# Performance work log

Measured on AMD Instinct MI355X. Metric: run time of the kernel, lower is better.

## Reference

```python
import jax, jax.numpy as jnp
import numpy as np

B = 524288
D_IN = 128
D_OUT = 128
MASK_DENSITY = 0.25  # fraction of DAG edges present


def setup_inputs() -> dict:
    key = jax.random.key(0)
    k = jax.random.split(key, 6)
    x0 = jax.random.normal(k[0], (B, D_IN), dtype=jnp.float32)
    x1 = jax.random.normal(k[1], (B, D_IN), dtype=jnp.float32)
    # weights ~ N(0, 0.1^2) as in torch.normal(mean=0, std=0.1)
    w0 = jax.random.normal(k[2], (D_OUT, D_IN), dtype=jnp.float32) * 0.1
    w1 = jax.random.normal(k[3], (D_OUT, D_IN), dtype=jnp.float32) * 0.1
    # binary DAG connectivity masks [out_dim, in_dims[i]]
    m0 = (jax.random.uniform(k[4], (D_OUT, D_IN)) < MASK_DENSITY).astype(jnp.float32)
    m1 = (jax.random.uniform(k[5], (D_OUT, D_IN)) < MASK_DENSITY).astype(jnp.float32)
    return {"x0": x0, "x1": x1, "w0": w0, "w1": w1, "m0": m0, "m1": m1}


def reference(x0, x1, w0, w1, m0, m1):
    # sum_i  x_i @ (W_i * M_i)^T   -> [B, out_dim]
    # (note: original module creates self.bias but never adds it in forward)
    out = jnp.einsum("bi,oi->bo", x0, w0 * m0)
    out = out + jnp.einsum("bi,oi->bo", x1, w1 * m1)
    return out
```

## Files before the change

### kernel.cpp

```cpp
#include <hip/hip_runtime.h>

typedef __attribute__((ext_vector_type(4))) float f32x4;
typedef __attribute__((ext_vector_type(4))) int   i32x4;
typedef __attribute__((ext_vector_type(2))) unsigned int u32x2;

#define NBLK 512
#define NTHR 512
#define NT   32
#define DOUT 128

__device__ __forceinline__ unsigned short bf_rne(float x) {
  unsigned u = __builtin_bit_cast(unsigned, x);
  return (unsigned short)((u + 0x7FFFu + ((u >> 16) & 1u)) >> 16);
}
__device__ __forceinline__ void split2(float x, short& hi, short& lo) {
  unsigned u = __builtin_bit_cast(unsigned, x);
  float hf = __builtin_bit_cast(float, u & 0xFFFF0000u);
  hi = (short)(unsigned short)(u >> 16);
  lo = (short)bf_rne(x - hf);
}
__device__ __forceinline__ unsigned cvtpk(float a, float b) {
  unsigned r;
  asm("v_cvt_pk_bf16_f32 %0, %1, %2" : "=v"(r) : "v"(a), "v"(b));
  return r;
}
__device__ __forceinline__ void gll16(const float* g, char* l) {
  __builtin_amdgcn_global_load_lds(
      (const __attribute__((address_space(1))) unsigned int*)g,
      (__attribute__((address_space(3))) unsigned int*)l, 16, 0, 0);
}
#define MFMA_AW(ACC, W, X)                                                   \
  asm("s_nop 1\n\tv_mfma_f32_16x16x32_bf16 %0, %1, %2, %0"                   \
      : "+v"(ACC) : "a"(W), "v"(X))

__global__ __launch_bounds__(NTHR, 2)
void dagmm(const float* __restrict__ x0, const float* __restrict__ x1,
           const float* __restrict__ w0, const float* __restrict__ w1,
           const float* __restrict__ m0, const float* __restrict__ m1,
           float* __restrict__ out)
{
  __shared__ __align__(16) char L[98304];
  const int t   = threadIdx.x;
  const int l   = t & 63;
  const int w   = t >> 6;
  const int l16 = l & 15;
  const int lq  = l >> 4;

  i32x4 WH[8], WL[8];
  {
    const int col = w * 16 + l16;
#pragma unroll
    for (int ks = 0; ks < 8; ++ks) {
      const int k0 = ks * 32 + lq * 8;
      const float* wp = (k0 < 128) ? (w0 + col * 128 + k0) : (w1 + col * 128 + (k0 - 128));
      const float* mp = (k0 < 128) ? (m0 + col * 128 + k0) : (m1 + col * 128 + (k0 - 128));
      float4 wa = *(const float4*)wp, wb = *(const float4*)(wp + 4);
      float4 ma = *(const float4*)mp, mb = *(const float4*)(mp + 4);
      float v[8] = {wa.x*ma.x, wa.y*ma.y, wa.z*ma.z, wa.w*ma.w,
                    wb.x*mb.x, wb.y*mb.y, wb.z*mb.z, wb.w*mb.w};
      short hv[8], lv[8];
#pragma unroll
      for (int j = 0; j < 8; ++j) split2(v[j], hv[j], lv[j]);
      WH[ks] = *(const i32x4*)hv;
      WL[ks] = *(const i32x4*)lv;
      asm volatile("" : "+a"(WH[ks]));
      asm volatile("" : "+a"(WL[ks]));
    }
  }

  const size_t Tbase = (size_t)blockIdx.x * (NT * 32);
  const float* xsrc = (l < 32) ? (x0 + l * 4) : (x1 + (l - 32) * 4);

#define ISSUE(ts, r)                                                         \
  {                                                                          \
    _Pragma("unroll")                                                        \
    for (int i = 0; i < 4; ++i) {                                            \
      const int row = w * 4 + i;                                             \
      const size_t grow = Tbase + (size_t)(ts) * 32 + row;                   \
      gll16(xsrc + grow * 128, L + (r) * 32768 + row * 1024);                \
    }                                                                        \
  }

  const int rowS = w * 4 + (l >> 4);
  const int vS   = l & 15;
#define SPLIT(r)                                                             \
  {                                                                          \
    const char* Fb = L + (r) * 32768 + rowS * 1024;                          \
    char*       Bb = L + 65536 + (r) * 16384 + (rowS >> 4) * 8192;           \
    _Pragma("unroll")                                                        \
    for (int q = 0; q < 4; ++q) {                                            \
      const int g = vS + 16 * q;               \
      f32x4 f = *(const f32x4*)(Fb + g * 16);                                \
      u32x2 hv;                                                              \
      hv[0] = cvtpk(f[0], f[1]);                                             \
      hv[1] = cvtpk(f[2], f[3]);                                             \
      const int ks   = g >> 3;                                               \
      const int lam  = (rowS & 15) | (((g >> 1) & 3) << 4);                  \
      char* p = Bb + ks * 1024 + ((lam ^ ks) << 4) + (g & 1) * 8;            \
      *(u32x2*)p = hv;                                                       \
    }                                                                        \
  }

  ISSUE(0, 0);
  ISSUE(1, 1);

  for (int tt = 0; tt < NT; ++tt) {
    const int r = tt & 1;

    asm volatile("s_waitcnt vmcnt(4)" ::: "memory");

    SPLIT(r);
    asm volatile("s_waitcnt lgkmcnt(0)" ::: "memory");
    __builtin_amdgcn_s_barrier();

    { const int ts = (tt + 2 < NT) ? (tt + 2) : (NT - 1); ISSUE(ts, r); }

    f32x4 acc0 = (f32x4){0.f, 0.f, 0.f, 0.f};
    f32x4 acc1 = (f32x4){0.f, 0.f, 0.f, 0.f};
    {
      const char* Bb = L + 65536 + r * 16384;
#pragma unroll
      for (int ks = 0; ks < 8; ++ks) {
        const char* p0 = Bb + ks * 1024 + ((l ^ ks) << 4);
        i32x4 xa = *(const i32x4*)p0;
        i32x4 xb = *(const i32x4*)(p0 + 8192);
        MFMA_AW(acc0, WH[ks], xa);
        MFMA_AW(acc1, WH[ks], xb);
        MFMA_AW(acc0, WL[ks], xa);
        MFMA_AW(acc1, WL[ks], xb);
      }
    }
    asm volatile("s_nop 7\n\ts_nop 7" :::);

    {
      const size_t row0 = Tbase + (size_t)tt * 32 + l16;
      *(f32x4*)&out[(row0     ) * DOUT + w * 16 + lq * 4] = acc0;
      *(f32x4*)&out[(row0 + 16) * DOUT + w * 16 + lq * 4] = acc1;
    }

    asm volatile("s_waitcnt lgkmcnt(0)" ::: "memory");
    __builtin_amdgcn_s_barrier();
  }
#undef ISSUE
#undef SPLIT
}

extern "C" void kernel_launch(void* const* d_in, const int* in_sizes, int n_in,
                              void* d_out, int out_size, void* d_ws, size_t ws_size,
                              hipStream_t stream) {
  const float* x0 = (const float*)d_in[0];
  const float* x1 = (const float*)d_in[1];
  const float* w0 = (const float*)d_in[2];
  const float* w1 = (const float*)d_in[3];
  const float* m0 = (const float*)d_in[4];
  const float* m1 = (const float*)d_in[5];
  dagmm<<<NBLK, NTHR, 0, stream>>>(x0, x1, w0, w1, m0, m1, (float*)d_out);
}
```

Baseline: 173.9 us.

## Replace LDS-DMA fp32 staging with register prefetch and 64-row tiles

Drops the global_load_lds path that staged fp32 x tiles in LDS before a separate bf16 split pass. Each thread now prefetches the next tile's x rows into registers, converts them to bf16 and writes them straight into a swizzled, double-buffered LDS tile. Tiles grow to 64 rows (NT halved), so each block does four MFMA row groups per iteration, and the second barrier per iteration is removed. This cuts LDS footprint and traffic, at the cost of more registers for the prefetch and only one tile of prefetch depth.

```diff
diff --git a/kernel.cpp b/kernel.cpp
--- a/kernel.cpp
+++ b/kernel.cpp
@@ -6,28 +6,20 @@
 
 #define NBLK 512
 #define NTHR 512
-#define NT   32
+#define NT   16
 #define DOUT 128
 
-__device__ __forceinline__ unsigned short bf_rne(float x) {
-  unsigned u = __builtin_bit_cast(unsigned, x);
-  return (unsigned short)((u + 0x7FFFu + ((u >> 16) & 1u)) >> 16);
-}
 __device__ __forceinline__ void split2(float x, short& hi, short& lo) {
   unsigned u = __builtin_bit_cast(unsigned, x);
   float hf = __builtin_bit_cast(float, u & 0xFFFF0000u);
   hi = (short)(unsigned short)(u >> 16);
-  lo = (short)bf_rne(x - hf);
+  unsigned v = __builtin_bit_cast(unsigned, x - hf);
+  lo = (short)(unsigned short)((v + 0x7FFFu + ((v >> 16) & 1u)) >> 16);
 }
 __device__ __forceinline__ unsigned cvtpk(float a, float b) {
   unsigned r;
   asm("v_cvt_pk_bf16_f32 %0, %1, %2" : "=v"(r) : "v"(a), "v"(b));
   return r;
-}
-__device__ __forceinline__ void gll16(const float* g, char* l) {
-  __builtin_amdgcn_global_load_lds(
-      (const __attribute__((address_space(1))) unsigned int*)g,
-      (__attribute__((address_space(3))) unsigned int*)l, 16, 0, 0);
 }
 #define MFMA_AW(ACC, W, X)                                                   \
   asm("s_nop 1\n\tv_mfma_f32_16x16x32_bf16 %0, %1, %2, %0"                   \
@@ -39,7 +31,8 @@
            const float* __restrict__ m0, const float* __restrict__ m1,
            float* __restrict__ out)
 {
-  __shared__ __align__(16) char L[98304];
+  __shared__ __align__(16) char L[65536];
+
   const int t   = threadIdx.x;
   const int l   = t & 63;
   const int w   = t >> 6;
@@ -68,81 +61,68 @@
     }
   }
 
-  const size_t Tbase = (size_t)blockIdx.x * (NT * 32);
-  const float* xsrc = (l < 32) ? (x0 + l * 4) : (x1 + (l - 32) * 4);
+  const size_t Tbase = (size_t)blockIdx.x * (NT * 64);
+  const float* xb = (l < 32) ? (x0 + l * 4) : (x1 + (l - 32) * 4);
 
-#define ISSUE(ts, r)                                                         \
+  float4 pf[8];
+#define LOADSTAGE(ts)                                                        \
   {                                                                          \
     _Pragma("unroll")                                                        \
-    for (int i = 0; i < 4; ++i) {                                            \
-      const int row = w * 4 + i;                                             \
-      const size_t grow = Tbase + (size_t)(ts) * 32 + row;                   \
-      gll16(xsrc + grow * 128, L + (r) * 32768 + row * 1024);                \
-    }                                                                        \
+    for (int s = 0; s < 8; ++s)                                              \
+      pf[s] = *(const float4*)(xb + (Tbase + (size_t)(ts) * 64 + w * 8 + s) * 128); \
   }
 
-  const int rowS = w * 4 + (l >> 4);
-  const int vS   = l & 15;
-#define SPLIT(r)                                                             \
+#define CVTWRITE(bb)                                                         \
   {                                                                          \
-    const char* Fb = L + (r) * 32768 + rowS * 1024;                          \
-    char*       Bb = L + 65536 + (r) * 16384 + (rowS >> 4) * 8192;           \
     _Pragma("unroll")                                                        \
-    for (int q = 0; q < 4; ++q) {                                            \
-      const int g = vS + 16 * q;               \
-      f32x4 f = *(const f32x4*)(Fb + g * 16);                                \
+    for (int s = 0; s < 8; ++s) {                                            \
+      const int row = w * 8 + s;                                             \
       u32x2 hv;                                                              \
-      hv[0] = cvtpk(f[0], f[1]);                                             \
-      hv[1] = cvtpk(f[2], f[3]);                                             \
-      const int ks   = g >> 3;                                               \
-      const int lam  = (rowS & 15) | (((g >> 1) & 3) << 4);                  \
-      char* p = Bb + ks * 1024 + ((lam ^ ks) << 4) + (g & 1) * 8;            \
+      hv[0] = cvtpk(pf[s].x, pf[s].y);                                       \
+      hv[1] = cvtpk(pf[s].z, pf[s].w);                                       \
+      const int f   = (row >> 4) * 8 + (l >> 3);                             \
+      const int lam = (row & 15) | (((l >> 1) & 3) << 4);                    \
+      char* p = L + (bb) + f * 1024 + ((lam ^ (f & 31)) << 4) + (l & 1) * 8; \
       *(u32x2*)p = hv;                                                       \
     }                                                                        \
   }
 
-  ISSUE(0, 0);
-  ISSUE(1, 1);
+  LOADSTAGE(0);
 
   for (int tt = 0; tt < NT; ++tt) {
-    const int r = tt & 1;
+    const int bb = (tt & 1) * 32768;
 
-    asm volatile("s_waitcnt vmcnt(4)" ::: "memory");
+    CVTWRITE(bb);
+    if (tt + 1 < NT) LOADSTAGE(tt + 1);
 
-    SPLIT(r);
     asm volatile("s_waitcnt lgkmcnt(0)" ::: "memory");
     __builtin_amdgcn_s_barrier();
+    asm volatile("" ::: "memory");
 
-    { const int ts = (tt + 2 < NT) ? (tt + 2) : (NT - 1); ISSUE(ts, r); }
-
-    f32x4 acc0 = (f32x4){0.f, 0.f, 0.f, 0.f};
-    f32x4 acc1 = (f32x4){0.f, 0.f, 0.f, 0.f};
-    {
-      const char* Bb = L + 65536 + r * 16384;
+    f32x4 acc[4];
 #pragma unroll
-      for (int ks = 0; ks < 8; ++ks) {
-        const char* p0 = Bb + ks * 1024 + ((l ^ ks) << 4);
-        i32x4 xa = *(const i32x4*)p0;
-        i32x4 xb = *(const i32x4*)(p0 + 8192);
-        MFMA_AW(acc0, WH[ks], xa);
-        MFMA_AW(acc1, WH[ks], xb);
-        MFMA_AW(acc0, WL[ks], xa);
-        MFMA_AW(acc1, WL[ks], xb);
+    for (int rt = 0; rt < 4; ++rt) acc[rt] = (f32x4){0.f, 0.f, 0.f, 0.f};
+#pragma unroll
+    for (int ks = 0; ks < 8; ++ks) {
+#pragma unroll
+      for (int rt = 0; rt < 4; ++rt) {
+        const int f = rt * 8 + ks;
+        const char* p = L + bb + f * 1024 + ((l ^ (f & 31)) << 4);
+        i32x4 xh = *(const i32x4*)p;
+        MFMA_AW(acc[rt], WH[ks], xh);
+        MFMA_AW(acc[rt], WL[ks], xh);
       }
     }
     asm volatile("s_nop 7\n\ts_nop 7" :::);
 
-    {
-      const size_t row0 = Tbase + (size_t)tt * 32 + l16;
-      *(f32x4*)&out[(row0     ) * DOUT + w * 16 + lq * 4] = acc0;
-      *(f32x4*)&out[(row0 + 16) * DOUT + w * 16 + lq * 4] = acc1;
+#pragma unroll
+    for (int rt = 0; rt < 4; ++rt) {
+      const size_t row = Tbase + (size_t)tt * 64 + rt * 16 + l16;
+      *(f32x4*)&out[row * DOUT + w * 16 + lq * 4] = acc[rt];
     }
-
-    asm volatile("s_waitcnt lgkmcnt(0)" ::: "memory");
-    __builtin_amdgcn_s_barrier();
   }
-#undef ISSUE
-#undef SPLIT
+#undef LOADSTAGE
+#undef CVTWRITE
 }
 
 extern "C" void kernel_launch(void* const* d_in, const int* in_sizes, int n_in,
```

After: 172.5 us. No clear change (-0.8%).
